# Performance work log

Measured on AMD Instinct MI355X. Metric: run time of the kernel, lower is better.

## Reference

```python
import jax, jax.numpy as jnp
import numpy as np

B = 4096          # batch_size
D_EMB = 16        # per-side embedding dim (embed_to_from width = 2*D_EMB)
D_HIGH = 784      # flattened high-dim feature size
NSR = 5           # negative_sample_rate
A = 1.576943      # UMAP _a
B_PARAM = 0.8950608  # UMAP _b
REPULSION = 1.0
EPS = 1e-4
GLOBAL_LOSS = 0.5
TOTAL_STEPS = 1000
BATCH_COUNT = 500  # fixed step for deterministic alpha/beta
WARMUP = int(0.05 * TOTAL_STEPS)


def _safe_sqrt(sq):
    # sqrt with zero (not NaN) gradient at 0, matching zero-distance pairs
    safe = jnp.where(sq > 0, sq, 1.0)
    return jnp.where(sq > 0, jnp.sqrt(safe), 0.0)


def _pairwise_dist(x):
    # ||x_i - x_j|| via gram trick; avoids materializing [N,N,D]
    sq = jnp.sum(x * x, axis=1)                      # [N]
    gram = x @ x.T                                   # [N,N]
    d2 = sq[:, None] + sq[None, :] - 2.0 * gram
    return _safe_sqrt(jnp.maximum(d2, 0.0))


def _umap_ce_loss(embed_to_from, perm):
    e_to, e_from = jnp.split(embed_to_from, 2, axis=1)   # [B, D_EMB] each
    neg_to = jnp.repeat(e_to, NSR, axis=0)               # [B*NSR, D_EMB]
    repeat_neg = jnp.repeat(e_from, NSR, axis=0)
    neg_from = repeat_neg[perm]                          # shuffled negatives
    d_pos = _safe_sqrt(jnp.sum((e_to - e_from) ** 2, axis=1))
    d_neg = _safe_sqrt(jnp.sum((neg_to - neg_from) ** 2, axis=1))
    dist = jnp.concatenate([d_pos, d_neg], axis=0)       # [B*(1+NSR)]
    p_dist = 1.0 / (1.0 + A * dist ** (2.0 * B_PARAM))
    p_graph = jnp.concatenate([jnp.ones(B, p_dist.dtype), jnp.zeros(B * NSR, p_dist.dtype)])
    attraction = -p_graph * jnp.log(jnp.clip(p_dist, EPS, 1.0))
    repellant = -(1.0 - p_graph) * jnp.log(jnp.clip(1.0 - p_dist, EPS, 1.0)) * REPULSION
    return jnp.mean(attraction + repellant)


def _global_feature_loss(embed_to_from, to_x):
    e_to = embed_to_from[:, :D_EMB]
    to_x = to_x.reshape(to_x.shape[0], -1)
    high_dis = _pairwise_dist(to_x)     # [N,N]
    low_dis = _pairwise_dist(e_to)      # [N,N]
    # row-wise pearson correlation between high_dis and low_dis
    h = high_dis - jnp.mean(high_dis, axis=1, keepdims=True)
    l = low_dis - jnp.mean(low_dis, axis=1, keepdims=True)
    num = jnp.sum(h * l, axis=1)
    den = jnp.sqrt(jnp.sum(h * h, axis=1)) * jnp.sqrt(jnp.sum(l * l, axis=1))
    corr = jnp.mean(num / den)
    return -corr


def _alpha_beta():
    if BATCH_COUNT >= WARMUP:
        if BATCH_COUNT <= 0.9 * TOTAL_STEPS:
            beta = max(0.0, GLOBAL_LOSS * (1 - BATCH_COUNT / (TOTAL_STEPS - WARMUP * 4)) ** 2)
        else:
            beta = 0.0
        alpha = max(0.0, 1 - beta)
    else:
        alpha = 0.0
        beta = GLOBAL_LOSS
    return alpha, beta


def setup_inputs() -> dict:
    key = jax.random.key(0)
    k1, k2, k3 = jax.random.split(key, 3)
    embed_to_from = jax.random.normal(k1, (B, 2 * D_EMB), dtype=jnp.float32)
    placeholder = jax.random.normal(k2, (B, D_HIGH), dtype=jnp.float32)
    perm = jax.random.permutation(k3, B * NSR).astype(jnp.int32)
    return {"embed_to_from": embed_to_from, "placeholder": placeholder, "perm": perm}


def reference(embed_to_from, placeholder, perm):
    loss = _umap_ce_loss(embed_to_from, perm)
    loss_g = _global_feature_loss(embed_to_from, placeholder)
    alpha, beta = _alpha_beta()
    return alpha * loss + beta * loss_g
```

## Files before the change

kernel.cpp:

```cpp
#include <hip/hip_runtime.h>
#include <hip/hip_bf16.h>
#include <math.h>

#define NB    4096
#define DH    784
#define KX8   832
#define NSR   5
#define NNEG  (NB*NSR)
#define NTOT  (NB + NNEG)

#define A_CONST 1.576943f
#define PEXP    1.7901216f
#define EPS_C   1.0e-4f
#define ALPHA_C 0.9296875f
#define BETA_C  0.0703125f

#define NSLOT 64
#define SLAB  (NB * NSLOT)
#define NBLK  528
#define BUFB  8192

typedef __hip_bfloat16 bf16;
typedef short bf16x8 __attribute__((ext_vector_type(8)));
typedef float f32x4  __attribute__((ext_vector_type(4)));
typedef float f32x2  __attribute__((ext_vector_type(2)));
typedef long long2v __attribute__((ext_vector_type(2)));

#define WS_XF8    0
#define WS_EBF    3407872
#define WS_SQX    3670016
#define WS_SQE    3686400
#define WS_STATSP 3702784
#define WS_UPART  8945664
#define WS_CPART  8946048
#define WS_CNT    8946304

__device__ __forceinline__ void gl2lds16(const void* g, void* l) {
    __builtin_amdgcn_global_load_lds(
        (const __attribute__((address_space(1))) unsigned int*)g,
        (__attribute__((address_space(3))) unsigned int*)l,
        16, 0, 0);
}

__global__ void prep_fused(const float* __restrict__ X, const float* __restrict__ emb,
                           const int* __restrict__ perm, unsigned char* __restrict__ Xf8,
                           float* __restrict__ sqx, bf16* __restrict__ Ebf,
                           float* __restrict__ sqe, float* __restrict__ upart,
                           unsigned* __restrict__ cnt) {
    if (blockIdx.x == 0 && threadIdx.x == 0) *cnt = 0u;
    if (blockIdx.x < 1024) {
        const int wave = threadIdx.x >> 6, lane = threadIdx.x & 63;
        const int row = blockIdx.x * 4 + wave;
        const float4* xr = (const float4*)(X + (size_t)row * DH);
        int* xb = (int*)(Xf8 + (size_t)row * KX8);
        float s = 0.f;
        #pragma unroll
        for (int it = 0; it < 4; ++it) {
            const int idx = lane + it * 64;
            if (idx < 208) {
                const int c = idx >> 4, p = idx & 15;
                const int q = p >> 2, h = (p >> 1) & 1, w = p & 1;
                const int src = c * 16 + h * 8 + q * 2 + w;
                int pk = 0;
                if (src < 196) {
                    float4 v = xr[src];
                    s += v.x * v.x + v.y * v.y + v.z * v.z + v.w * v.w;
                    int lo = __builtin_amdgcn_cvt_pk_fp8_f32(v.x, v.y, 0, false);
                    pk = __builtin_amdgcn_cvt_pk_fp8_f32(v.z, v.w, lo, true);
                }
                xb[idx] = pk;
            }
        }
        #pragma unroll
        for (int off = 32; off; off >>= 1) s += __shfl_down(s, off, 64);
        if (lane == 0) sqx[row] = s;
        return;
    }
    const int ub = blockIdx.x - 1024;
    const int t = ub * 256 + threadIdx.x;
    float val = 0.f;
    if (t < NB) {
        const float4* av = (const float4*)(emb + (size_t)t * 32);
        float4 t0 = av[0], t1 = av[1], t2 = av[2], t3 = av[3];
        float4 f0 = av[4], f1 = av[5], f2 = av[6], f3 = av[7];
        bf16* eb = Ebf + (size_t)t * 32;
        union { bf16 h[4]; ushort4 u; } cv;
        #define ST4(dst, q) cv.h[0]=__float2bfloat16(q.x); cv.h[1]=__float2bfloat16(q.y); \
                            cv.h[2]=__float2bfloat16(q.z); cv.h[3]=__float2bfloat16(q.w); \
                            *(ushort4*)(dst) = cv.u;
        ST4(eb,      t0) ST4(eb + 4,  t1) ST4(eb + 8,  t2) ST4(eb + 12, t3)
        #undef ST4
        ushort4 z = {0, 0, 0, 0};
        *(ushort4*)(eb + 16) = z; *(ushort4*)(eb + 20) = z;
        *(ushort4*)(eb + 24) = z; *(ushort4*)(eb + 28) = z;
        sqe[t] = t0.x*t0.x + t0.y*t0.y + t0.z*t0.z + t0.w*t0.w
               + t1.x*t1.x + t1.y*t1.y + t1.z*t1.z + t1.w*t1.w
               + t2.x*t2.x + t2.y*t2.y + t2.z*t2.z + t2.w*t2.w
               + t3.x*t3.x + t3.y*t3.y + t3.z*t3.z + t3.w*t3.w;
        float d2 = 0.f;
        #define D2(a, b) { float4 df = {a.x-b.x, a.y-b.y, a.z-b.z, a.w-b.w}; \
                           d2 += df.x*df.x + df.y*df.y + df.z*df.z + df.w*df.w; }
        D2(t0, f0) D2(t1, f1) D2(t2, f2) D2(t3, f3)
        #undef D2
        float d = sqrtf(d2);
        float p = 1.f / (1.f + A_CONST * powf(d, PEXP));
        val = -logf(fminf(fmaxf(p, EPS_C), 1.f));
    } else if (t < NTOT) {
        const int k = t - NB;
        const int ti = k / 5;
        const int fi = perm[k] / 5;
        const float4* at = (const float4*)(emb + (size_t)ti * 32);
        const float4* bt = (const float4*)(emb + (size_t)fi * 32 + 16);
        float d2 = 0.f;
        #pragma unroll
        for (int q = 0; q < 4; ++q) {
            float4 a = at[q], b = bt[q];
            float4 df = {a.x-b.x, a.y-b.y, a.z-b.z, a.w-b.w};
            d2 += df.x*df.x + df.y*df.y + df.z*df.z + df.w*df.w;
        }
        float d = sqrtf(d2);
        float p = 1.f / (1.f + A_CONST * powf(d, PEXP));
        val = -logf(fminf(fmaxf(1.f - p, EPS_C), 1.f));
    }
    #pragma unroll
    for (int off = 32; off; off >>= 1) val += __shfl_down(val, off, 64);
    __shared__ float ps[4];
    if ((threadIdx.x & 63) == 0) ps[threadIdx.x >> 6] = val;
    __syncthreads();
    if (threadIdx.x == 0) upart[ub] = ps[0] + ps[1] + ps[2] + ps[3];
}

__global__ __launch_bounds__(512, 4) void gram_kernel(
    const unsigned char* __restrict__ Xf8, const bf16* __restrict__ Ebf,
    const float* __restrict__ sqx, const float* __restrict__ sqe,
    float* __restrict__ statsp) {
    __shared__ __align__(16) unsigned char smem[67584];
    unsigned char* As = smem;
    unsigned char* Bs = smem + 4 * BUFB;
    float* sqxs = (float*)(smem + 65536);
    float* sqes = (float*)(smem + 66560);
    float* scr  = (float*)smem;

#define BARLDS() do { asm volatile("s_waitcnt lgkmcnt(0)" ::: "memory"); \
                      __builtin_amdgcn_s_barrier(); } while (0)

    int bi, bj;
    {
        const int k = blockIdx.x & 7;
        const int idx = blockIdx.x >> 3;
        int g = -1, r = 0;
        if (k < 6) {
            const int SG[6] = {0,0,0,1,1,2}, SH[6] = {1,2,3,2,3,3};
            if (idx < 64) { bi = SG[k]*8 + (idx>>3); bj = SH[k]*8 + (idx&7); }
            else {
                const int DG[6] = {1,0,3,1,3,3};
                const int DR[6] = {32,34,30,34,32,34};
                g = DG[k]; r = DR[k] + (idx - 64);
            }
        } else if (k == 6) {
            if (idx < 34) { g = 0; r = idx; } else { g = 1; r = idx - 34; }
        } else {
            if (idx < 36) { g = 2; r = idx; } else { g = 3; r = idx - 36; }
        }
        if (g >= 0) {
            int a = 0;
            while (r >= 8 - a) { r -= 8 - a; ++a; }
            bi = g * 8 + a; bj = g * 8 + a + r;
        }
    }
    const int i0 = bi * 128, j0 = bj * 128;

    const int tid  = threadIdx.x;
    const int wave = tid >> 6;
    const int lane = tid & 63;
    const int wy = wave >> 1, wx = wave & 1;
    const int quad = lane >> 4, l15 = lane & 15;

    f32x4 acc[2][4];
    #pragma unroll
    for (int a = 0; a < 2; ++a)
        #pragma unroll
        for (int b = 0; b < 4; ++b)
            acc[a][b] = (f32x4){0.f, 0.f, 0.f, 0.f};

    const int rA  = lane >> 2;
    const int gsb = (((lane & 3) ^ ((lane >> 3) & 3))) * 16;
    const unsigned char* gA = Xf8 + (size_t)(i0 + wave * 16 + rA) * KX8 + gsb;
    const unsigned char* gB = Xf8 + (size_t)(j0 + wave * 16 + rA) * KX8 + gsb;

    if (tid < 128) {
        sqxs[tid] = sqx[i0 + tid]; sqxs[128 + tid] = sqx[j0 + tid];
        sqes[tid] = sqe[i0 + tid]; sqes[128 + tid] = sqe[j0 + tid];
    }
    __syncthreads();

    #pragma unroll
    for (int s = 0; s < 3; ++s) {
        gl2lds16(gA, As + s * BUFB + wave * 1024);
        gl2lds16(gB, Bs + s * BUFB + wave * 1024);
        gA += 64; gB += 64;
    }

    const int key = (l15 >> 1) & 3;
    const int boX = ((quad ^ key) << 4);

    #pragma unroll
    for (int t = 0; t < 13; ++t) {
        if (t < 12) { asm volatile("s_waitcnt vmcnt(4)" ::: "memory"); }
        else        { asm volatile("s_waitcnt vmcnt(2)" ::: "memory"); }
        __builtin_amdgcn_s_barrier();
        const int cur = (t & 3) * BUFB;
        const int nb  = ((t + 3) & 3) * BUFB;
        if (t < 10) {
            gl2lds16(gA, As + nb + wave * 1024);
            gl2lds16(gB, Bs + nb + wave * 1024);
            gA += 64; gB += 64;
        } else if (t == 10) {
            gl2lds16((const unsigned char*)(Ebf + (size_t)(i0 + wave * 16 + rA) * 32) + gsb,
                     As + BUFB + wave * 1024);
            gl2lds16((const unsigned char*)(Ebf + (size_t)(j0 + wave * 16 + rA) * 32) + gsb,
                     Bs + BUFB + wave * 1024);
        }
        long2v aF[2], bF[4];
        #pragma unroll
        for (int mi = 0; mi < 2; ++mi)
            aF[mi] = *(const long2v*)&As[cur + (wy * 32 + mi * 16 + l15) * 64 + boX];
        #pragma unroll
        for (int ni = 0; ni < 4; ++ni)
            bF[ni] = *(const long2v*)&Bs[cur + (wx * 64 + ni * 16 + l15) * 64 + boX];
        #pragma unroll
        for (int mi = 0; mi < 2; ++mi)
            #pragma unroll
            for (int ni = 0; ni < 4; ++ni) {
                acc[mi][ni] = __builtin_amdgcn_mfma_f32_16x16x32_fp8_fp8(
                    aF[mi][0], bF[ni][0], acc[mi][ni], 0, 0, 0);
                acc[mi][ni] = __builtin_amdgcn_mfma_f32_16x16x32_fp8_fp8(
                    aF[mi][1], bF[ni][1], acc[mi][ni], 0, 0, 0);
            }
    }
    asm volatile("s_waitcnt vmcnt(0)" ::: "memory");
    __builtin_amdgcn_s_barrier();

    bf16x8 afE[2], bfrE[4];
    #pragma unroll
    for (int mi = 0; mi < 2; ++mi)
        afE[mi] = *(const bf16x8*)&As[BUFB + (wy * 32 + mi * 16 + l15) * 64 + boX];
    #pragma unroll
    for (int ni = 0; ni < 4; ++ni)
        bfrE[ni] = *(const bf16x8*)&Bs[BUFB + (wx * 64 + ni * 16 + l15) * 64 + boX];
    float sqxj[4], sqej[4];
    #pragma unroll
    for (int ni = 0; ni < 4; ++ni) {
        const int jl = wx * 64 + ni * 16 + l15;
        sqxj[ni] = sqxs[128 + jl]; sqej[ni] = sqes[128 + jl];
    }
    BARLDS();

    float cst[4][5];
    #pragma unroll
    for (int ni = 0; ni < 4; ++ni)
        #pragma unroll
        for (int c = 0; c < 5; ++c) cst[ni][c] = 0.f;

    #pragma unroll
    for (int mi = 0; mi < 2; ++mi) {
        f32x4 aE[4];
        #pragma unroll
        for (int ni = 0; ni < 4; ++ni) {
            f32x4 z = (f32x4){0.f, 0.f, 0.f, 0.f};
            aE[ni] = __builtin_amdgcn_mfma_f32_16x16x32_bf16(afE[mi], bfrE[ni], z, 0, 0, 0);
        }
        const int ilb = wy * 32 + mi * 16 + quad * 4;
        float sqxi[4], sqei[4];
        #pragma unroll
        for (int r = 0; r < 4; ++r) { sqxi[r] = sqxs[ilb + r]; sqei[r] = sqes[ilb + r]; }
        float rs[5][4];
        #pragma unroll
        for (int c = 0; c < 5; ++c)
            #pragma unroll
            for (int r = 0; r < 4; ++r) rs[c][r] = 0.f;
        #pragma unroll
        for (int ni = 0; ni < 4; ++ni) {
            const int j = j0 + wx * 64 + ni * 16 + l15;
            #pragma unroll
            for (int r = 0; r < 4; ++r) {
                const int i = i0 + ilb + r;
                float H, L;
                if (i == j) { H = 0.f; L = 0.f; }
                else {
                    float d2  = sqxi[r] + sqxj[ni] - 2.0f * acc[mi][ni][r];
                    H = sqrtf(fmaxf(d2, 0.f));
                    float d2e = sqei[r] + sqej[ni] - 2.0f * aE[ni][r];
                    L = sqrtf(fmaxf(d2e, 0.f));
                }
                rs[0][r] += H; rs[1][r] += H * H; rs[2][r] += L;
                rs[3][r] += L * L; rs[4][r] += H * L;
                cst[ni][0] += H; cst[ni][1] += H * H; cst[ni][2] += L;
                cst[ni][3] += L * L; cst[ni][4] += H * L;
            }
        }
        #pragma unroll
        for (int c = 0; c < 5; ++c)
            #pragma unroll
            for (int r = 0; r < 4; ++r)
                scr[(size_t)((((wx * 5 + c) << 6) + (wy << 4) + (quad << 2) + r)) * 18 + l15]
                    = rs[c][r];
        BARLDS();
        for (int o = tid; o < 640; o += 512) {
            const int wxo = (o >= 320) ? 1 : 0;
            const int rem = o - wxo * 320;
            const int c = rem >> 6, li = rem & 63;
            const float* p = scr + (size_t)(((wxo * 5 + c) << 6) + li) * 18;
            float s = 0.f;
            #pragma unroll
            for (int k = 0; k < 16; k += 2) { f32x2 v = *(const f32x2*)&p[k]; s += v.x + v.y; }
            const int iloc = ((li >> 4) << 5) + mi * 16 + (li & 15);
            statsp[(size_t)c * SLAB + (size_t)(bj * 2 + wxo) * NB + (i0 + iloc)] = s;
        }
        BARLDS();
    }

    if (bi != bj) {
        #pragma unroll
        for (int ni = 0; ni < 4; ++ni) {
            const int jl = wx * 64 + ni * 16 + l15;
            #pragma unroll
            for (int c = 0; c < 5; ++c)
                scr[(size_t)(c * 128 + jl) * 17 + (wy << 2) + quad] = cst[ni][c];
        }
        BARLDS();
        for (int o = tid; o < 1280; o += 512) {
            const int c = o >> 8, h = (o >> 7) & 1, j = o & 127;
            const float* p = scr + (size_t)(c * 128 + j) * 17 + h * 8;
            float s = ((p[0] + p[1]) + (p[2] + p[3])) + ((p[4] + p[5]) + (p[6] + p[7]));
            statsp[(size_t)c * SLAB + (size_t)(bi * 2 + h) * NB + (j0 + j)] = s;
        }
    }
#undef BARLDS
}

__global__ void finish1_kernel(const float* __restrict__ statsp, const float* __restrict__ upart,
                               float* __restrict__ cpart, unsigned* __restrict__ cnt,
                               float* __restrict__ out) {
    __shared__ float ps2[4][64][5];
    const int t = threadIdx.x;
    const int rloc = t & 63;
    const int sg = t >> 6;
    const int r = blockIdx.x * 64 + rloc;
    float sh = 0.f, sh2 = 0.f, sl = 0.f, sl2 = 0.f, shl = 0.f;
    for (int s = sg * 16; s < sg * 16 + 16; ++s) {
        const float* base = statsp + (size_t)s * NB + r;
        sh  += base[0 * SLAB];
        sh2 += base[1 * SLAB];
        sl  += base[2 * SLAB];
        sl2 += base[3 * SLAB];
        shl += base[4 * SLAB];
    }
    ps2[sg][rloc][0] = sh; ps2[sg][rloc][1] = sh2; ps2[sg][rloc][2] = sl;
    ps2[sg][rloc][3] = sl2; ps2[sg][rloc][4] = shl;
    __syncthreads();
    if (t < 64) {
        float a = 0.f, b = 0.f, c = 0.f, d = 0.f, e = 0.f;
        #pragma unroll
        for (int g = 0; g < 4; ++g) {
            a += ps2[g][t][0]; b += ps2[g][t][1]; c += ps2[g][t][2];
            d += ps2[g][t][3]; e += ps2[g][t][4];
        }
        const float invN = 1.0f / (float)NB;
        float num = e - a * c * invN;
        float vh  = fmaxf(b - a * a * invN, 0.f);
        float vl  = fmaxf(d - c * c * invN, 0.f);
        float local = num / (sqrtf(vh) * sqrtf(vl));
        #pragma unroll
        for (int off = 32; off; off >>= 1) local += __shfl_down(local, off, 64);
        if (t == 0) cpart[blockIdx.x] = local;
    }
    __shared__ int lastFlag;
    if (t == 0) {
        __threadfence();
        unsigned prev = atomicAdd(cnt, 1u);
        lastFlag = (prev == 63u);
    }
    __syncthreads();
    if (lastFlag) {
        __threadfence();
        float v = 0.f;
        if (t < 64) v += cpart[t] * (-BETA_C / (float)NB);
        if (t < 96) v += upart[t] * (ALPHA_C / (float)NTOT);
        #pragma unroll
        for (int off = 32; off; off >>= 1) v += __shfl_down(v, off, 64);
        __shared__ float fin[4];
        if ((t & 63) == 0) fin[t >> 6] = v;
        __syncthreads();
        if (t == 0) out[0] = fin[0] + fin[1] + fin[2] + fin[3];
    }
}

extern "C" void kernel_launch(void* const* d_in, const int* in_sizes, int n_in,
                              void* d_out, int out_size, void* d_ws, size_t ws_size,
                              hipStream_t stream) {
    const float* emb  = (const float*)d_in[0];
    const float* ph   = (const float*)d_in[1];
    const int*   perm = (const int*)d_in[2];
    float* out = (float*)d_out;

    char* ws = (char*)d_ws;
    unsigned char* Xf8 = (unsigned char*)(ws + WS_XF8);
    bf16*  Ebf    = (bf16*) (ws + WS_EBF);
    float* sqx    = (float*)(ws + WS_SQX);
    float* sqe    = (float*)(ws + WS_SQE);
    float* statsp = (float*)(ws + WS_STATSP);
    float* upart  = (float*)(ws + WS_UPART);
    float* cpart  = (float*)(ws + WS_CPART);
    unsigned* cnt = (unsigned*)(ws + WS_CNT);

    prep_fused<<<1120, 256, 0, stream>>>(ph, emb, perm, Xf8, sqx, Ebf, sqe, upart, cnt);
    gram_kernel<<<NBLK, 512, 0, stream>>>(Xf8, Ebf, sqx, sqe, statsp);
    finish1_kernel<<<64, 256, 0, stream>>>(statsp, upart, cpart, cnt, out);
}
```

Baseline: 121.9 us.

## Fuse final correlation reduction into gram kernel via atomic row accumulators

```diff
diff --git a/kernel.cpp b/kernel.cpp
--- a/kernel.cpp
+++ b/kernel.cpp
@@ -15,8 +15,6 @@
 #define ALPHA_C 0.9296875f
 #define BETA_C  0.0703125f
 
-#define NSLOT 64
-#define SLAB  (NB * NSLOT)
 #define NBLK  528
 #define BUFB  8192
 
@@ -30,9 +28,8 @@
 #define WS_EBF    3407872
 #define WS_SQX    3670016
 #define WS_SQE    3686400
-#define WS_STATSP 3702784
+#define WS_ACC5   3702784
 #define WS_UPART  8945664
-#define WS_CPART  8946048
 #define WS_CNT    8946304
 
 __device__ __forceinline__ void gl2lds16(const void* g, void* l) {
@@ -46,7 +43,7 @@
                            const int* __restrict__ perm, unsigned char* __restrict__ Xf8,
                            float* __restrict__ sqx, bf16* __restrict__ Ebf,
                            float* __restrict__ sqe, float* __restrict__ upart,
-                           unsigned* __restrict__ cnt) {
+                           float* __restrict__ acc5, unsigned* __restrict__ cnt) {
     if (blockIdx.x == 0 && threadIdx.x == 0) *cnt = 0u;
     if (blockIdx.x < 1024) {
         const int wave = threadIdx.x >> 6, lane = threadIdx.x & 63;
@@ -78,6 +75,7 @@
     }
     const int ub = blockIdx.x - 1024;
     const int t = ub * 256 + threadIdx.x;
+    if (t < 5 * NB) acc5[t] = 0.f;
     float val = 0.f;
     if (t < NB) {
         const float4* av = (const float4*)(emb + (size_t)t * 32);
@@ -133,7 +131,8 @@
 __global__ __launch_bounds__(512, 4) void gram_kernel(
     const unsigned char* __restrict__ Xf8, const bf16* __restrict__ Ebf,
     const float* __restrict__ sqx, const float* __restrict__ sqe,
-    float* __restrict__ statsp) {
+    float* __restrict__ acc5, const float* __restrict__ upart,
+    unsigned* __restrict__ cnt, float* __restrict__ out) {
     __shared__ __align__(16) unsigned char smem[67584];
     unsigned char* As = smem;
     unsigned char* Bs = smem + 4 * BUFB;
@@ -306,16 +305,18 @@
                 scr[(size_t)((((wx * 5 + c) << 6) + (wy << 4) + (quad << 2) + r)) * 18 + l15]
                     = rs[c][r];
         BARLDS();
-        for (int o = tid; o < 640; o += 512) {
-            const int wxo = (o >= 320) ? 1 : 0;
-            const int rem = o - wxo * 320;
-            const int c = rem >> 6, li = rem & 63;
-            const float* p = scr + (size_t)(((wxo * 5 + c) << 6) + li) * 18;
+        for (int o = tid; o < 320; o += 512) {
+            const int c = o >> 6, li = o & 63;
+            const float* p0 = scr + (size_t)((c << 6) + li) * 18;
+            const float* p1 = scr + (size_t)(((5 + c) << 6) + li) * 18;
             float s = 0.f;
             #pragma unroll
-            for (int k = 0; k < 16; k += 2) { f32x2 v = *(const f32x2*)&p[k]; s += v.x + v.y; }
+            for (int k = 0; k < 16; k += 2) {
+                f32x2 v0 = *(const f32x2*)&p0[k]; s += v0.x + v0.y;
+                f32x2 v1 = *(const f32x2*)&p1[k]; s += v1.x + v1.y;
+            }
             const int iloc = ((li >> 4) << 5) + mi * 16 + (li & 15);
-            statsp[(size_t)c * SLAB + (size_t)(bj * 2 + wxo) * NB + (i0 + iloc)] = s;
+            unsafeAtomicAdd(&acc5[(size_t)c * NB + (i0 + iloc)], s);
         }
         BARLDS();
     }
@@ -329,71 +330,52 @@
                 scr[(size_t)(c * 128 + jl) * 17 + (wy << 2) + quad] = cst[ni][c];
         }
         BARLDS();
-        for (int o = tid; o < 1280; o += 512) {
-            const int c = o >> 8, h = (o >> 7) & 1, j = o & 127;
-            const float* p = scr + (size_t)(c * 128 + j) * 17 + h * 8;
-            float s = ((p[0] + p[1]) + (p[2] + p[3])) + ((p[4] + p[5]) + (p[6] + p[7]));
-            statsp[(size_t)c * SLAB + (size_t)(bi * 2 + h) * NB + (j0 + j)] = s;
-        }
-    }
-#undef BARLDS
-}
-
-__global__ void finish1_kernel(const float* __restrict__ statsp, const float* __restrict__ upart,
-                               float* __restrict__ cpart, unsigned* __restrict__ cnt,
-                               float* __restrict__ out) {
-    __shared__ float ps2[4][64][5];
-    const int t = threadIdx.x;
-    const int rloc = t & 63;
-    const int sg = t >> 6;
-    const int r = blockIdx.x * 64 + rloc;
-    float sh = 0.f, sh2 = 0.f, sl = 0.f, sl2 = 0.f, shl = 0.f;
-    for (int s = sg * 16; s < sg * 16 + 16; ++s) {
-        const float* base = statsp + (size_t)s * NB + r;
-        sh  += base[0 * SLAB];
-        sh2 += base[1 * SLAB];
-        sl  += base[2 * SLAB];
-        sl2 += base[3 * SLAB];
-        shl += base[4 * SLAB];
-    }
-    ps2[sg][rloc][0] = sh; ps2[sg][rloc][1] = sh2; ps2[sg][rloc][2] = sl;
-    ps2[sg][rloc][3] = sl2; ps2[sg][rloc][4] = shl;
+        for (int o = tid; o < 640; o += 512) {
+            const int c = o >> 7, j = o & 127;
+            const float* p = scr + (size_t)(c * 128 + j) * 17;
+            float s = (((p[0] + p[1]) + (p[2] + p[3])) + ((p[4] + p[5]) + (p[6] + p[7])))
+                    + (((p[8] + p[9]) + (p[10] + p[11])) + ((p[12] + p[13]) + (p[14] + p[15])));
+            unsafeAtomicAdd(&acc5[(size_t)c * NB + (j0 + j)], s);
+        }
+    }
+
+    __shared__ int lastFlag;
     __syncthreads();
-    if (t < 64) {
-        float a = 0.f, b = 0.f, c = 0.f, d = 0.f, e = 0.f;
-        #pragma unroll
-        for (int g = 0; g < 4; ++g) {
-            a += ps2[g][t][0]; b += ps2[g][t][1]; c += ps2[g][t][2];
-            d += ps2[g][t][3]; e += ps2[g][t][4];
-        }
-        const float invN = 1.0f / (float)NB;
-        float num = e - a * c * invN;
-        float vh  = fmaxf(b - a * a * invN, 0.f);
-        float vl  = fmaxf(d - c * c * invN, 0.f);
-        float local = num / (sqrtf(vh) * sqrtf(vl));
-        #pragma unroll
-        for (int off = 32; off; off >>= 1) local += __shfl_down(local, off, 64);
-        if (t == 0) cpart[blockIdx.x] = local;
-    }
-    __shared__ int lastFlag;
-    if (t == 0) {
+    if (tid == 0) {
         __threadfence();
-        unsigned prev = atomicAdd(cnt, 1u);
-        lastFlag = (prev == 63u);
+        lastFlag = (atomicAdd(cnt, 1u) == (unsigned)(NBLK - 1));
     }
     __syncthreads();
     if (lastFlag) {
         __threadfence();
+        const float invN = 1.0f / (float)NB;
         float v = 0.f;
-        if (t < 64) v += cpart[t] * (-BETA_C / (float)NB);
-        if (t < 96) v += upart[t] * (ALPHA_C / (float)NTOT);
+        #pragma unroll
+        for (int rr = 0; rr < 8; ++rr) {
+            const int r = tid + rr * 512;
+            const float a  = acc5[0 * NB + r];
+            const float b  = acc5[1 * NB + r];
+            const float c2 = acc5[2 * NB + r];
+            const float d  = acc5[3 * NB + r];
+            const float e  = acc5[4 * NB + r];
+            float num = e - a * c2 * invN;
+            float vh  = fmaxf(b - a * a * invN, 0.f);
+            float vl  = fmaxf(d - c2 * c2 * invN, 0.f);
+            v += num / (sqrtf(vh) * sqrtf(vl));
+        }
+        v *= (-BETA_C * invN);
+        if (tid < 96) v += upart[tid] * (ALPHA_C / (float)NTOT);
         #pragma unroll
         for (int off = 32; off; off >>= 1) v += __shfl_down(v, off, 64);
-        __shared__ float fin[4];
-        if ((t & 63) == 0) fin[t >> 6] = v;
+        float* fin = (float*)smem;
         __syncthreads();
-        if (t == 0) out[0] = fin[0] + fin[1] + fin[2] + fin[3];
-    }
+        if ((tid & 63) == 0) fin[tid >> 6] = v;
+        __syncthreads();
+        if (tid == 0)
+            out[0] = ((fin[0] + fin[1]) + (fin[2] + fin[3]))
+                   + ((fin[4] + fin[5]) + (fin[6] + fin[7]));
+    }
+#undef BARLDS
 }
 
 extern "C" void kernel_launch(void* const* d_in, const int* in_sizes, int n_in,
@@ -409,12 +391,10 @@
     bf16*  Ebf    = (bf16*) (ws + WS_EBF);
     float* sqx    = (float*)(ws + WS_SQX);
     float* sqe    = (float*)(ws + WS_SQE);
-    float* statsp = (float*)(ws + WS_STATSP);
+    float* acc5   = (float*)(ws + WS_ACC5);
     float* upart  = (float*)(ws + WS_UPART);
-    float* cpart  = (float*)(ws + WS_CPART);
     unsigned* cnt = (unsigned*)(ws + WS_CNT);
 
-    prep_fused<<<1120, 256, 0, stream>>>(ph, emb, perm, Xf8, sqx, Ebf, sqe, upart, cnt);
-    gram_kernel<<<NBLK, 512, 0, stream>>>(Xf8, Ebf, sqx, sqe, statsp);
-    finish1_kernel<<<64, 256, 0, stream>>>(statsp, upart, cpart, cnt, out);
+    prep_fused<<<1120, 256, 0, stream>>>(ph, emb, perm, Xf8, sqx, Ebf, sqe, upart, acc5, cnt);
+    gram_kernel<<<NBLK, 512, 0, stream>>>(Xf8, Ebf, sqx, sqe, acc5, upart, cnt, out);
 }
```

Result: faster. 111.1 us (-8.9%).
